# Kernel tuning notes

Measured on AMD Instinct MI355X. Metric: run time of the kernel, lower is better.

The kernel has to match this reference:

```python
import math
import jax, jax.numpy as jnp
import numpy as np

L = 3
EPS = 1e-06


def _geometry(H, W, L):
    """Replicates the Python-side region layout of the torch ramac() exactly."""
    ovr = 0.4
    steps = np.array([2, 3, 4, 5, 6, 7], dtype=np.float64)
    w = min(W, H)
    b = (max(H, W) - w) / (steps - 1)
    idx = int(np.argmin(np.abs((w ** 2 - w * b) / w ** 2 - ovr)))
    Wd = idx if H < W else 0
    Hd = idx if H > W else 0
    regions = []  # list of (i, j, wl) static ints
    for l in range(1, L + 1):
        wl = math.floor(2 * w / (l + 1))
        if wl == 0:
            continue
        wl2 = math.floor(wl / 2 - 1)
        bW = 0 if l + Wd == 1 else (W - wl) / (l + Wd - 1)
        cenW = [int(math.floor(wl2 + k * bW) - wl2) for k in range(l - 1 + Wd + 1)]
        bH = 0 if l + Hd == 1 else (H - wl) / (l + Hd - 1)
        cenH = [int(math.floor(wl2 + k * bH) - wl2) for k in range(l - 1 + Hd + 1)]
        for i in cenH:
            for j in cenW:
                regions.append((i, j, wl))
    return regions


def _weighted_mac(R, tt_region, eps):
    # R: [B, C, h, w]; tt_region: [B, h, w] bool
    vt = R.max(axis=(2, 3))  # [B, C] regional max-pool
    area = tt_region.shape[-2] * tt_region.shape[-1]
    # NOTE: faithful to torch: sum over batch too, divided only by region area
    wgt = tt_region.sum().astype(jnp.float32) / area
    wgt = jnp.where(wgt <= 1.0 / 3.0, jnp.zeros_like(wgt), wgt)
    nrm = jnp.linalg.norm(vt, axis=1, keepdims=True)  # L2 over channels
    return vt / (nrm + eps) * wgt


def _ramac(x, L, eps):
    B, C, H, W = x.shape
    s = x.sum(axis=1)                 # [B, H, W]
    tt = (s - s.mean()) > 0           # [B, H, W] attention mask (bool)
    v = _weighted_mac(x, tt, eps)     # global region
    for (i, j, wl) in _geometry(H, W, L):
        R = x[:, :, i:i + wl, j:j + wl]
        v = v + _weighted_mac(R, tt[:, i:i + wl, j:j + wl], eps)
    return v.reshape(B, C, 1, 1)


def setup_inputs() -> dict:
    key = jax.random.key(0)
    x = jax.random.normal(key, (16, 1024, 64, 64), dtype=jnp.float32)
    return {"x": x}


def reference(x):
    return _ramac(x, L, EPS)
```

## Files before the change

kernel.cpp:

```cpp
#include <hip/hip_runtime.h>
#include <math.h>


#define NB 16
#define NC 1024
#define G 32
#define NCHUNK (NC / G)

template <int ctrl, int rm, int bm>
__device__ __forceinline__ float maxdpp(float x) {
  int xi = __float_as_int(x);
  int yi = __builtin_amdgcn_update_dpp(xi, xi, ctrl, rm, bm, false);
  return fmaxf(x, __int_as_float(yi));
}
__device__ __forceinline__ float wave_max64(float x) {
  x = maxdpp<0x111, 0xf, 0xf>(x);
  x = maxdpp<0x112, 0xf, 0xf>(x);
  x = maxdpp<0x114, 0xf, 0xe>(x);
  x = maxdpp<0x118, 0xf, 0xc>(x);
  x = maxdpp<0x142, 0xa, 0xf>(x);
  x = maxdpp<0x143, 0x8, 0xf>(x);
  return x;
}

__global__ __launch_bounds__(256) void k1_main(
    const float4* __restrict__ x, float4* __restrict__ vtp4,
    float4* __restrict__ spart4, float* __restrict__ total,
    int* __restrict__ cnt) {
  const int t = threadIdx.x;
  const int chunk = blockIdx.x;
  const int b = blockIdx.y;
  if (chunk == 0 && b == 0) {
    if (t == 0) *total = 0.f;
    if (t < 14) cnt[t] = 0;
  }
  const int fb = t & 15;
  const int r0t = t >> 4;
  const int w = t >> 6;
  const float NEG = -INFINITY;
  const bool cAf = (fb <= 9), cAp = (fb == 10);
  const bool cBf = (fb >= 6), cBp = (fb == 5);
  const bool cCm = (fb < 8);
  const bool cDm = (fb >= 4) && (fb < 12);
  const bool cEm = (fb >= 8);
  const bool rAk2 = (r0t < 10);
  const bool rBk1 = (r0t >= 6);

  __shared__ float4 sm4[14][G];

  float4 sa0 = {0, 0, 0, 0}, sa1 = {0, 0, 0, 0}, sa2 = {0, 0, 0, 0},
         sa3 = {0, 0, 0, 0};
  const float4* img = x + (((size_t)(b * NC + chunk * G)) << 10);

  auto process = [&](float4 v0, float4 v1, float4 v2, float4 v3, int ci) {
    sa0.x += v0.x; sa0.y += v0.y; sa0.z += v0.z; sa0.w += v0.w;
    sa1.x += v1.x; sa1.y += v1.y; sa1.z += v1.z; sa1.w += v1.w;
    sa2.x += v2.x; sa2.y += v2.y; sa2.z += v2.z; sa2.w += v2.w;
    sa3.x += v3.x; sa3.y += v3.y; sa3.z += v3.z; sa3.w += v3.w;

    float m0 = fmaxf(fmaxf(v0.x, v0.y), fmaxf(v0.z, v0.w));
    float m1 = fmaxf(fmaxf(v1.x, v1.y), fmaxf(v1.z, v1.w));
    float m2 = fmaxf(fmaxf(v2.x, v2.y), fmaxf(v2.z, v2.w));
    float m3 = fmaxf(fmaxf(v3.x, v3.y), fmaxf(v3.z, v3.w));
    float pA0 = fmaxf(v0.x, v0.y), pA1 = fmaxf(v1.x, v1.y);
    float pA2 = fmaxf(v2.x, v2.y), pA3 = fmaxf(v3.x, v3.y);
    float pB0 = fmaxf(v0.z, v0.w), pB1 = fmaxf(v1.z, v1.w);
    float pB2 = fmaxf(v2.z, v2.w), pB3 = fmaxf(v3.z, v3.w);

    float m01 = fmaxf(m0, m1), m12 = fmaxf(m1, m2), m23 = fmaxf(m2, m3);
    float MAm = fmaxf(m01, rAk2 ? m2 : NEG);
    float MBm = fmaxf(m23, rBk1 ? m1 : NEG);
    float MApA = fmaxf(fmaxf(pA0, pA1), rAk2 ? pA2 : NEG);
    float MApB = fmaxf(fmaxf(pB0, pB1), rAk2 ? pB2 : NEG);
    float MBpA = fmaxf(fmaxf(pA2, pA3), rBk1 ? pA1 : NEG);
    float MBpB = fmaxf(fmaxf(pB2, pB3), rBk1 ? pB1 : NEG);

    float g0 = fmaxf(m01, m23);
    float g1 = cAf ? MAm : (cAp ? MApA : NEG);
    float g2 = cBf ? MAm : (cBp ? MApB : NEG);
    float g3 = cAf ? MBm : (cAp ? MBpA : NEG);
    float g4 = cBf ? MBm : (cBp ? MBpB : NEG);
    float g5 = cCm ? m01 : NEG, g6 = cDm ? m01 : NEG, g7 = cEm ? m01 : NEG;
    float g8 = cCm ? m12 : NEG, g9 = cDm ? m12 : NEG, g10 = cEm ? m12 : NEG;
    float g11 = cCm ? m23 : NEG, g12 = cDm ? m23 : NEG, g13 = cEm ? m23 : NEG;

    g0 = wave_max64(g0);   g1 = wave_max64(g1);   g2 = wave_max64(g2);
    g3 = wave_max64(g3);   g4 = wave_max64(g4);   g5 = wave_max64(g5);
    g6 = wave_max64(g6);   g7 = wave_max64(g7);   g8 = wave_max64(g8);
    g9 = wave_max64(g9);   g10 = wave_max64(g10); g11 = wave_max64(g11);
    g12 = wave_max64(g12); g13 = wave_max64(g13);

    if ((t & 63) == 63) {
      float* smf = (float*)&sm4[0][0];
      const int o = (ci << 2) + w;
      smf[o]               = g0;  smf[o + 1 * (G * 4)] = g1;
      smf[o + 2 * (G * 4)] = g2;  smf[o + 3 * (G * 4)] = g3;
      smf[o + 4 * (G * 4)] = g4;  smf[o + 5 * (G * 4)] = g5;
      smf[o + 6 * (G * 4)] = g6;  smf[o + 7 * (G * 4)] = g7;
      smf[o + 8 * (G * 4)] = g8;  smf[o + 9 * (G * 4)] = g9;
      smf[o + 10 * (G * 4)] = g10; smf[o + 11 * (G * 4)] = g11;
      smf[o + 12 * (G * 4)] = g12; smf[o + 13 * (G * 4)] = g13;
    }
  };

  float4 v0 = img[t], v1 = img[t + 256], v2 = img[t + 512], v3 = img[t + 768];
  for (int ci = 0; ci < G - 1; ++ci) {
    const float4* q = img + (((size_t)(ci + 1)) << 10);
    float4 n0 = q[t], n1 = q[t + 256], n2 = q[t + 512], n3 = q[t + 768];
    process(v0, v1, v2, v3, ci);
    v0 = n0; v1 = n1; v2 = n2; v3 = n3;
  }
  process(v0, v1, v2, v3, G - 1);

  const int sb = ((chunk * NB + b) << 10);
  spart4[sb + t] = sa0;
  spart4[sb + t + 256] = sa1;
  spart4[sb + t + 512] = sa2;
  spart4[sb + t + 768] = sa3;

  __syncthreads();
  for (int i = t; i < 14 * G; i += 256) {
    const int r = i / G, ci = i % G;
    vtp4[r * (NB * NC) + (b << 10) + chunk * G + ci] = sm4[r][ci];
  }
}

__global__ __launch_bounds__(256) void k2_mid(
    const float4* __restrict__ spart4, float4* __restrict__ s4,
    float* __restrict__ total, const float4* __restrict__ vtp4,
    float* __restrict__ vt, float* __restrict__ nrm) {
  const int blk = blockIdx.x;
  const int t = threadIdx.x;
  __shared__ float red[4];
  if (blk < 64) {
    const int id = blk * 256 + t;
    float4 acc = {0, 0, 0, 0};
    for (int ch = 0; ch < NCHUNK; ++ch) {
      float4 v = spart4[(ch << 14) + id];
      acc.x += v.x; acc.y += v.y; acc.z += v.z; acc.w += v.w;
    }
    s4[id] = acc;
    float ts = (acc.x + acc.y) + (acc.z + acc.w);
    for (int off = 1; off < 64; off <<= 1) ts += __shfl_xor(ts, off);
    if ((t & 63) == 0) atomicAdd(total, ts);
  } else {
    const int rb = blk - 64;
    float acc = 0.f;
#pragma unroll
    for (int k = 0; k < 4; ++k) {
      const int c = t + 256 * k;
      float4 v = vtp4[(rb << 10) + c];
      float m = fmaxf(fmaxf(v.x, v.y), fmaxf(v.z, v.w));
      vt[(rb << 10) + c] = m;
      acc += m * m;
    }
    for (int off = 1; off < 64; off <<= 1) acc += __shfl_xor(acc, off);
    if ((t & 63) == 0) red[t >> 6] = acc;
    __syncthreads();
    if (t == 0) nrm[rb] = sqrtf(red[0] + red[1] + red[2] + red[3]);
  }
}

__global__ __launch_bounds__(256) void k3_cnt(const float* __restrict__ s,
                                              const float* __restrict__ total,
                                              int* __restrict__ cnt) {
  const int b = blockIdx.x;
  const int t = threadIdx.x;
  const float mean = *total * (1.0f / 65536.0f);
  int loc[14];
#pragma unroll
  for (int r = 0; r < 14; ++r) loc[r] = 0;
#pragma unroll
  for (int k = 0; k < 16; ++k) {
    const int p = t + 256 * k;
    const int row = p >> 6, col = p & 63;
    const bool tt = s[(b << 12) + p] > mean;
    if (tt) {
      const bool rA = row < 42, rB = row >= 22, rC = row < 32;
      const bool rD = (row >= 16) && (row < 48), rE = row >= 32;
      const bool cA = col < 42, cB = col >= 22, cC = col < 32;
      const bool cD = (col >= 16) && (col < 48), cE = col >= 32;
      loc[0]++;
      loc[1] += rA && cA;  loc[2] += rA && cB;
      loc[3] += rB && cA;  loc[4] += rB && cB;
      loc[5] += rC && cC;  loc[6] += rC && cD;  loc[7] += rC && cE;
      loc[8] += rD && cC;  loc[9] += rD && cD;  loc[10] += rD && cE;
      loc[11] += rE && cC; loc[12] += rE && cD; loc[13] += rE && cE;
    }
  }
#pragma unroll
  for (int r = 0; r < 14; ++r) {
    int v = loc[r];
    for (int off = 1; off < 64; off <<= 1) v += __shfl_xor(v, off);
    if ((t & 63) == 0) atomicAdd(&cnt[r], v);
  }
}

__global__ __launch_bounds__(256) void k4_out(const float* __restrict__ vt,
                                              const float* __restrict__ nrm,
                                              const int* __restrict__ cnt,
                                              float* __restrict__ out) {
  const int id = blockIdx.x * 256 + threadIdx.x;
  const int b = id >> 10;
  float acc = 0.f;
#pragma unroll
  for (int r = 0; r < 14; ++r) {
    const float area = (r == 0) ? 4096.f : ((r <= 4) ? 1764.f : 1024.f);
    float wgt = (float)cnt[r] / area;
    if (wgt <= (1.0f / 3.0f)) wgt = 0.f;
    const float mult = (r == 0) ? 2.f : 1.f;
    acc += mult * wgt * vt[r * 16384 + id] / (nrm[r * 16 + b] + 1e-6f);
  }
  out[id] = acc;
}

extern "C" void kernel_launch(void* const* d_in, const int* in_sizes, int n_in,
                              void* d_out, int out_size, void* d_ws,
                              size_t ws_size, hipStream_t stream) {
  const float* x = (const float*)d_in[0];
  float* out = (float*)d_out;

  float* ws = (float*)d_ws;
  float* vtp = ws;
  float* spart = vtp + 917504;
  float* s = spart + 2097152;
  float* vt = s + 65536;
  float* nrm = vt + 229376;
  float* total = nrm + 224;
  int* cnt = (int*)(total + 1);

  k1_main<<<dim3(NCHUNK, NB), 256, 0, stream>>>(
      (const float4*)x, (float4*)vtp, (float4*)spart, total, cnt);
  k2_mid<<<64 + 224, 256, 0, stream>>>((const float4*)spart, (float4*)s, total,
                                       (const float4*)vtp, vt, nrm);
  k3_cnt<<<NB, 256, 0, stream>>>(s, total, cnt);
  k4_out<<<64, 256, 0, stream>>>(vt, nrm, cnt, out);
}
```

Baseline: 385.3 us.

## Halve channel chunk size, share partial max reductions, split count kernel

Reduces channels per block from 32 to 16, doubling the k1 grid to 1024 blocks for better occupancy (launch bounds now request 4 blocks per CU). The nine level-3 region max reductions are replaced by three shared shuffle/DPP chains whose partial results are read from specific lanes, cutting cross-lane reduction instructions per channel. The count kernel is split across 4 blocks per batch for more parallelism. The cost is that spart doubles in size, so k2 has to read twice as many partial-sum chunks.

```diff
diff --git a/kernel.cpp b/kernel.cpp
--- a/kernel.cpp
+++ b/kernel.cpp
@@ -4,7 +4,7 @@
 
 #define NB 16
 #define NC 1024
-#define G 32
+#define G 16
 #define NCHUNK (NC / G)
 
 template <int ctrl, int rm, int bm>
@@ -22,8 +22,11 @@
   x = maxdpp<0x143, 0x8, 0xf>(x);
   return x;
 }
-
-__global__ __launch_bounds__(256) void k1_main(
+__device__ __forceinline__ float shflxor_max(float x, int m) {
+  return fmaxf(x, __shfl_xor(x, m));
+}
+
+__global__ __launch_bounds__(256, 4) void k1_main(
     const float4* __restrict__ x, float4* __restrict__ vtp4,
     float4* __restrict__ spart4, float* __restrict__ total,
     int* __restrict__ cnt) {
@@ -37,12 +40,10 @@
   const int fb = t & 15;
   const int r0t = t >> 4;
   const int w = t >> 6;
+  const int L = t & 63;
   const float NEG = -INFINITY;
   const bool cAf = (fb <= 9), cAp = (fb == 10);
   const bool cBf = (fb >= 6), cBp = (fb == 5);
-  const bool cCm = (fb < 8);
-  const bool cDm = (fb >= 4) && (fb < 12);
-  const bool cEm = (fb >= 8);
   const bool rAk2 = (r0t < 10);
   const bool rBk1 = (r0t >= 6);
 
@@ -51,6 +52,15 @@
   float4 sa0 = {0, 0, 0, 0}, sa1 = {0, 0, 0, 0}, sa2 = {0, 0, 0, 0},
          sa3 = {0, 0, 0, 0};
   const float4* img = x + (((size_t)(b * NC + chunk * G)) << 10);
+
+  auto chain = [&](float V, float& outCE, float& outD) {
+    float a = shflxor_max(V, 16);
+    a = shflxor_max(a, 32);
+    float b4 = maxdpp<0xB1, 0xf, 0xf>(a);
+    b4 = maxdpp<0x4E, 0xf, 0xf>(b4);
+    outD = fmaxf(b4, __shfl_xor(b4, 12));
+    outCE = maxdpp<0x141, 0xf, 0xf>(b4);
+  };
 
   auto process = [&](float4 v0, float4 v1, float4 v2, float4 v3, int ci) {
     sa0.x += v0.x; sa0.y += v0.y; sa0.z += v0.z; sa0.w += v0.w;
@@ -80,26 +90,30 @@
     float g2 = cBf ? MAm : (cBp ? MApB : NEG);
     float g3 = cAf ? MBm : (cAp ? MBpA : NEG);
     float g4 = cBf ? MBm : (cBp ? MBpB : NEG);
-    float g5 = cCm ? m01 : NEG, g6 = cDm ? m01 : NEG, g7 = cEm ? m01 : NEG;
-    float g8 = cCm ? m12 : NEG, g9 = cDm ? m12 : NEG, g10 = cEm ? m12 : NEG;
-    float g11 = cCm ? m23 : NEG, g12 = cDm ? m23 : NEG, g13 = cEm ? m23 : NEG;
-
-    g0 = wave_max64(g0);   g1 = wave_max64(g1);   g2 = wave_max64(g2);
-    g3 = wave_max64(g3);   g4 = wave_max64(g4);   g5 = wave_max64(g5);
-    g6 = wave_max64(g6);   g7 = wave_max64(g7);   g8 = wave_max64(g8);
-    g9 = wave_max64(g9);   g10 = wave_max64(g10); g11 = wave_max64(g11);
-    g12 = wave_max64(g12); g13 = wave_max64(g13);
-
-    if ((t & 63) == 63) {
-      float* smf = (float*)&sm4[0][0];
-      const int o = (ci << 2) + w;
-      smf[o]               = g0;  smf[o + 1 * (G * 4)] = g1;
-      smf[o + 2 * (G * 4)] = g2;  smf[o + 3 * (G * 4)] = g3;
-      smf[o + 4 * (G * 4)] = g4;  smf[o + 5 * (G * 4)] = g5;
-      smf[o + 6 * (G * 4)] = g6;  smf[o + 7 * (G * 4)] = g7;
-      smf[o + 8 * (G * 4)] = g8;  smf[o + 9 * (G * 4)] = g9;
-      smf[o + 10 * (G * 4)] = g10; smf[o + 11 * (G * 4)] = g11;
-      smf[o + 12 * (G * 4)] = g12; smf[o + 13 * (G * 4)] = g13;
+    g0 = wave_max64(g0); g1 = wave_max64(g1); g2 = wave_max64(g2);
+    g3 = wave_max64(g3); g4 = wave_max64(g4);
+
+    float ceC, dC, ceD, dD, ceE, dE;
+    chain(m01, ceC, dC);
+    chain(m12, ceD, dD);
+    chain(m23, ceE, dE);
+
+    float* smf = (float*)&sm4[0][0];
+    const int o = (ci << 2) + w;
+    const int RS = G * 4;
+    if (L == 63) {
+      smf[o]          = g0;  smf[o + 1 * RS] = g1;
+      smf[o + 2 * RS] = g2;  smf[o + 3 * RS] = g3;
+      smf[o + 4 * RS] = g4;
+    }
+    if (L == 0) {
+      smf[o + 5 * RS] = ceC; smf[o + 8 * RS] = ceD; smf[o + 11 * RS] = ceE;
+    }
+    if (L == 4) {
+      smf[o + 6 * RS] = dC;  smf[o + 9 * RS] = dD;  smf[o + 12 * RS] = dE;
+    }
+    if (L == 8) {
+      smf[o + 7 * RS] = ceC; smf[o + 10 * RS] = ceD; smf[o + 13 * RS] = ceE;
     }
   };
 
@@ -120,7 +134,7 @@
 
   __syncthreads();
   for (int i = t; i < 14 * G; i += 256) {
-    const int r = i / G, ci = i % G;
+    const int r = i >> 4, ci = i & 15;
     vtp4[r * (NB * NC) + (b << 10) + chunk * G + ci] = sm4[r][ci];
   }
 }
@@ -164,15 +178,16 @@
 __global__ __launch_bounds__(256) void k3_cnt(const float* __restrict__ s,
                                               const float* __restrict__ total,
                                               int* __restrict__ cnt) {
-  const int b = blockIdx.x;
+  const int b = blockIdx.x >> 2;
+  const int q = blockIdx.x & 3;
   const int t = threadIdx.x;
   const float mean = *total * (1.0f / 65536.0f);
   int loc[14];
 #pragma unroll
   for (int r = 0; r < 14; ++r) loc[r] = 0;
 #pragma unroll
-  for (int k = 0; k < 16; ++k) {
-    const int p = t + 256 * k;
+  for (int k = 0; k < 4; ++k) {
+    const int p = t + 256 * (q * 4 + k);
     const int row = p >> 6, col = p & 63;
     const bool tt = s[(b << 12) + p] > mean;
     if (tt) {
@@ -223,7 +238,7 @@
   float* ws = (float*)d_ws;
   float* vtp = ws;
   float* spart = vtp + 917504;
-  float* s = spart + 2097152;
+  float* s = spart + 4194304;
   float* vt = s + 65536;
   float* nrm = vt + 229376;
   float* total = nrm + 224;
@@ -233,6 +248,6 @@
       (const float4*)x, (float4*)vtp, (float4*)spart, total, cnt);
   k2_mid<<<64 + 224, 256, 0, stream>>>((const float4*)spart, (float4*)s, total,
                                        (const float4*)vtp, vt, nrm);
-  k3_cnt<<<NB, 256, 0, stream>>>(s, total, cnt);
+  k3_cnt<<<64, 256, 0, stream>>>(s, total, cnt);
   k4_out<<<64, 256, 0, stream>>>(vt, nrm, cnt, out);
 }
```

New measurement: 413.0 us. +7.2%, slower.
